# Optimization experiments

Measured on AMD Instinct MI355X. Metric: run time of the kernel, lower is better.

## Reference

```python
import jax, jax.numpy as jnp
import numpy as np

N = 50000          # nodes
E = 800000         # edges (COO)
IN_CH = 128
H1, H2, OUT = 200, 100, 2   # 100*out, 50*out, out with out_channels=2
EPS = 1e-12
DROP_P = 0.1


def setup_inputs() -> dict:
    key = jax.random.key(0)
    ks = jax.random.split(key, 6)
    x = jax.random.normal(ks[0], (N, IN_CH), dtype=jnp.float32)
    edge_index = jax.random.randint(ks[1], (2, E), 0, N)
    W1 = jax.random.normal(ks[2], (IN_CH, H1), dtype=jnp.float32) / np.sqrt(IN_CH)
    W2 = jax.random.normal(ks[3], (H1, H2), dtype=jnp.float32) / np.sqrt(H1)
    W3 = jax.random.normal(ks[4], (H2, OUT), dtype=jnp.float32) / np.sqrt(H2)
    beta1 = jnp.float32(1.0)
    beta2 = jnp.float32(1.0)
    beta3 = jnp.float32(1.0)
    return dict(x=x, edge_index=edge_index, W1=W1, W2=W2, W3=W3,
                beta1=beta1, beta2=beta2, beta3=beta3)


def _agnn_layer(x, W, beta, src, dst):
    # project in -> out channels, then AGNN cosine-attention propagation
    h = x @ W                                               # [N, D]
    hn = h / jnp.maximum(jnp.linalg.norm(h, axis=-1, keepdims=True), EPS)
    a = beta * jnp.sum(hn[src] * hn[dst], axis=-1)          # [E'] edge logits
    amax = jax.ops.segment_max(a, dst, num_segments=N)      # stable segment softmax
    amax = jnp.where(jnp.isfinite(amax), amax, 0.0)
    e = jnp.exp(a - amax[dst])
    denom = jax.ops.segment_sum(e, dst, num_segments=N)
    alpha = e / jnp.maximum(denom[dst], EPS)
    return jax.ops.segment_sum(h[src] * alpha[:, None], dst, num_segments=N)


def _dropout(k, x, p=DROP_P):
    keep = jax.random.bernoulli(k, 1.0 - p, x.shape)
    return jnp.where(keep, x / (1.0 - p), 0.0)


def reference(x, edge_index, W1, W2, W3, beta1, beta2, beta3):
    src, dst = edge_index[0], edge_index[1]
    loop = jnp.arange(N)                                    # self-loops (AGNNConv default)
    src = jnp.concatenate([src, loop])
    dst = jnp.concatenate([dst, loop])
    k1, k2 = jax.random.split(jax.random.key(42))
    h = jax.nn.relu(_agnn_layer(x, W1, beta1, src, dst))
    h = _dropout(k1, h)
    h = jax.nn.relu(_agnn_layer(h, W2, beta2, src, dst))
    h = _dropout(k2, h)
    h = jax.nn.relu(_agnn_layer(h, W3, beta3, src, dst))
    return h
```

## Files before the change

kernel.cpp:

```cpp
#include <hip/hip_runtime.h>
#include <hip/hip_bf16.h>

#define NN 50000
#define NE 800000
#define EPSN 1e-12f


#define H_OFF    0ull
#define A_OFF    40000000ull
#define H3_OFF   80000000ull
#define RINV_OFF 80400000ull
#define OFFS_OFF 80600000ull
#define DEG_OFF  80800016ull
#define CURS_OFF 81000016ull
#define ESRC_OFF 81200016ull
#define CHNK_OFF 84600016ull

__host__ __device__ inline void tf20(unsigned k0, unsigned k1, unsigned& x0, unsigned& x1) {
  unsigned ks2 = k0 ^ k1 ^ 0x1BD11BDAu;
  x0 += k0; x1 += k1;
#define TFR(r) { x0 += x1; x1 = ((x1 << (r)) | (x1 >> (32 - (r)))) ^ x0; }
  TFR(13) TFR(15) TFR(26) TFR(6)
  x0 += k1;  x1 += ks2 + 1u;
  TFR(17) TFR(29) TFR(16) TFR(24)
  x0 += ks2; x1 += k0 + 2u;
  TFR(13) TFR(15) TFR(26) TFR(6)
  x0 += k0;  x1 += k1 + 3u;
  TFR(17) TFR(29) TFR(16) TFR(24)
  x0 += k1;  x1 += ks2 + 4u;
  TFR(13) TFR(15) TFR(26) TFR(6)
  x0 += ks2; x1 += k0 + 5u;
#undef TFR
}

__device__ __forceinline__ float dropf(float val, unsigned k0, unsigned k1, unsigned i) {
  unsigned x0 = 0u, x1 = i;
  tf20(k0, k1, x0, x1);
  unsigned bits = x0 ^ x1;
  float u = __uint_as_float((bits >> 9) | 0x3F800000u) - 1.0f;
  return (u < 0.9f) ? val * (1.0f / 0.9f) : 0.0f;
}

__device__ __forceinline__ float wave_sum(float x) {
  x += __shfl_xor(x, 32); x += __shfl_xor(x, 16); x += __shfl_xor(x, 8);
  x += __shfl_xor(x, 4);  x += __shfl_xor(x, 2);  x += __shfl_xor(x, 1);
  return x;
}

template<int K, int KT, int NLP, int N>
__device__ __forceinline__ void gemm_core(float* __restrict__ As, float* __restrict__ Ws,
                                          const float* __restrict__ A,
                                          const float* __restrict__ W,
                                          float* __restrict__ H,
                                          float* __restrict__ RINV, int M, int row0) {
  static_assert(NLP % 32 == 0, "NLP must be 32-granular");
  constexpr int KTP = KT + 1, NV = N / 4, NC = NLP / 32, CPT = NC * 4;
  const float4* A4 = (const float4*)A;
  const float4* W4 = (const float4*)W;
  const float4* Ws4 = (const float4*)Ws;

  int t = threadIdx.x, rgrp = t >> 3, cg = t & 7;
  float acc0[CPT], acc1[CPT];
#pragma unroll
  for (int j = 0; j < CPT; j++) { acc0[j] = 0.f; acc1[j] = 0.f; }

  for (int k0 = 0; k0 < K; k0 += KT) {
    __syncthreads();
    for (int idx = t; idx < 64 * (KT / 4); idx += 256) {
      int r = idx / (KT / 4), cq = idx - r * (KT / 4);
      int gr = row0 + r;
      float4 v = (gr < M) ? A4[(size_t)gr * (K / 4) + (k0 / 4) + cq]
                          : make_float4(0.f, 0.f, 0.f, 0.f);
      float* dst = &As[r * KTP + cq * 4];
      dst[0] = v.x; dst[1] = v.y; dst[2] = v.z; dst[3] = v.w;
    }
    for (int idx = t; idx < KT * NV; idx += 256) {
      int kk = idx / NV, cq = idx - kk * NV;
      *(float4*)&Ws[kk * NLP + cq * 4] = W4[(size_t)(k0 + kk) * NV + cq];
    }
    if (NLP > N) {
      for (int idx = t; idx < KT * ((NLP - N) / 4); idx += 256) {
        int kk = idx / ((NLP - N) / 4), cq = idx - kk * ((NLP - N) / 4);
        *(float4*)&Ws[kk * NLP + N + cq * 4] = make_float4(0.f, 0.f, 0.f, 0.f);
      }
    }
    __syncthreads();
#pragma unroll
    for (int kk = 0; kk < KT; kk++) {
      float a0 = As[(rgrp * 2) * KTP + kk];
      float a1 = As[(rgrp * 2 + 1) * KTP + kk];
#pragma unroll
      for (int q = 0; q < NC; q++) {
        float4 wv = Ws4[kk * (NLP / 4) + cg + 8 * q];
        acc0[q * 4 + 0] = fmaf(a0, wv.x, acc0[q * 4 + 0]);
        acc0[q * 4 + 1] = fmaf(a0, wv.y, acc0[q * 4 + 1]);
        acc0[q * 4 + 2] = fmaf(a0, wv.z, acc0[q * 4 + 2]);
        acc0[q * 4 + 3] = fmaf(a0, wv.w, acc0[q * 4 + 3]);
        acc1[q * 4 + 0] = fmaf(a1, wv.x, acc1[q * 4 + 0]);
        acc1[q * 4 + 1] = fmaf(a1, wv.y, acc1[q * 4 + 1]);
        acc1[q * 4 + 2] = fmaf(a1, wv.z, acc1[q * 4 + 2]);
        acc1[q * 4 + 3] = fmaf(a1, wv.w, acc1[q * 4 + 3]);
      }
    }
  }

  int r0 = row0 + rgrp * 2;
#pragma unroll
  for (int rr = 0; rr < 2; rr++) {
    int gr = r0 + rr;
    const float* acc = rr ? acc1 : acc0;
    float ss = 0.f;
#pragma unroll
    for (int q = 0; q < NC; q++) {
#pragma unroll
      for (int j = 0; j < 4; j++) {
        float v = acc[q * 4 + j];
        ss += v * v;
        int c = 4 * (cg + 8 * q) + j;
        if (gr < M && c < N) H[(size_t)gr * N + c] = v;
      }
    }
    ss += __shfl_xor(ss, 1); ss += __shfl_xor(ss, 2); ss += __shfl_xor(ss, 4);
    if (cg == 0 && gr < M) RINV[gr] = 1.0f / fmaxf(sqrtf(ss), EPSN);
  }
}

__global__ __launch_bounds__(256) void gemm1_hist_kernel(
    const float* __restrict__ X, const float* __restrict__ W1,
    float* __restrict__ H, float* __restrict__ RINV,
    const int* __restrict__ EI, int* __restrict__ DEG) {
  __shared__ float smem[9280];
  int bid = blockIdx.x;
  if (bid < 782) {
    gemm_core<128, 32, 224, 200>(smem, smem + 2112, X, W1, H, RINV, NN, bid * 64);
  } else {
    for (int e = (bid - 782) * 256 + threadIdx.x; e < NE; e += 242 * 256)
      atomicAdd(&DEG[EI[NE + e]], 1);
  }
}

__global__ __launch_bounds__(256) void csr_scan1_kernel(const int* __restrict__ deg,
                                                        int* __restrict__ offs,
                                                        int* __restrict__ chunk) {
  __shared__ int lds[8];
  int t = threadIdx.x;
  int base = blockIdx.x * 1024 + t * 4;
  int d[4];
#pragma unroll
  for (int j = 0; j < 4; j++) d[j] = (base + j < NN) ? deg[base + j] : 0;
  int ts = d[0] + d[1] + d[2] + d[3];
  int lane = t & 63, wave = t >> 6;
  int inc = ts;
#pragma unroll
  for (int sh = 1; sh < 64; sh <<= 1) { int u = __shfl_up(inc, sh); if (lane >= sh) inc += u; }
  if (lane == 63) lds[wave] = inc;
  __syncthreads();
  if (t == 0) { int s = 0; for (int w = 0; w < 4; w++) { int x = lds[w]; lds[w] = s; s += x; } lds[4] = s; }
  __syncthreads();
  int p = lds[wave] + inc - ts;
#pragma unroll
  for (int j = 0; j < 4; j++) { if (base + j < NN) offs[base + j] = p; p += d[j]; }
  if (t == 255) chunk[blockIdx.x] = lds[4];
}

__global__ __launch_bounds__(64) void csr_scan2_kernel(int* __restrict__ chunk) {
  int t = threadIdx.x;
  int v = (t < 49) ? chunk[t] : 0;
  int inc = v;
#pragma unroll
  for (int sh = 1; sh < 64; sh <<= 1) { int u = __shfl_up(inc, sh); if (t >= sh) inc += u; }
  if (t < 49) chunk[t] = inc - v;
}

__global__ __launch_bounds__(256) void csr_scan3_kernel(int* __restrict__ offs,
                                                        const int* __restrict__ chunk,
                                                        int* __restrict__ curs) {
  int i = blockIdx.x * 256 + threadIdx.x;
  if (i < NN) {
    int val = offs[i] + chunk[i >> 10];
    offs[i] = val;
    curs[i] = val;
  }
  if (i == 0) offs[NN] = NE;
}

__global__ __launch_bounds__(256) void csr_scatter_kernel(const int* __restrict__ ei,
                                                          int* __restrict__ curs,
                                                          int* __restrict__ esrc) {
  int e = blockIdx.x * 256 + threadIdx.x;
  if (e >= NE) return;
  int s = ei[e], d = ei[NE + e];
  int pos = atomicAdd(&curs[d], 1);
  esrc[pos] = s;
}

__global__ __launch_bounds__(256) void gemm2_kernel(const float* A, const float* W,
                                                    float* H, float* RINV, int M) {
  __shared__ float As[64 * 41];
  __shared__ float Ws[40 * 128];
  gemm_core<200, 40, 128, 100>(As, Ws, A, W, H, RINV, M, blockIdx.x * 64);
}

template<int D, int VEC, bool DROP>
__device__ __forceinline__ void attn_body(const float* __restrict__ H,
                                          const float* __restrict__ RINV,
                                          const int* __restrict__ OFFS,
                                          const int* __restrict__ ESRC,
                                          const float* __restrict__ BETA,
                                          float* __restrict__ OUT,
                                          unsigned k0, unsigned k1) {
  constexpr int NL = D / VEC;
  int v = blockIdx.x * 4 + (threadIdx.x >> 6);
  int lane = threadIdx.x & 63;
  bool act = lane < NL;
  float beta = BETA[0];
  float bd = beta * RINV[v];
  int e0 = OFFS[v], e1 = OFFS[v + 1];

  float wself = __expf(beta);
  float s = wself;
  float hd[VEC], acc[VEC];
  if (act) {
    const float* hrow = H + (size_t)v * D + lane * VEC;
    if (VEC == 4) { float4 tv = *(const float4*)hrow; hd[0] = tv.x; hd[1] = tv.y; hd[2] = tv.z; hd[3] = tv.w; }
    else          { float2 tv = *(const float2*)hrow; hd[0] = tv.x; hd[1] = tv.y; }
#pragma unroll
    for (int j = 0; j < VEC; j++) acc[j] = wself * hd[j];
  }

  int idx = e0;
  for (; idx + 4 <= e1; idx += 4) {
    int   u[4];
    float r[4], dt[4], hs[4][VEC];
#pragma unroll
    for (int m = 0; m < 4; m++) u[m] = ESRC[idx + m];
#pragma unroll
    for (int m = 0; m < 4; m++) r[m] = RINV[u[m]];
    float dd[4] = {0.f, 0.f, 0.f, 0.f};
    if (act) {
#pragma unroll
      for (int m = 0; m < 4; m++) {
        const float* p = H + (size_t)u[m] * D + lane * VEC;
        if (VEC == 4) { float4 a = *(const float4*)p; hs[m][0] = a.x; hs[m][1] = a.y; hs[m][2] = a.z; hs[m][3] = a.w; }
        else          { float2 a = *(const float2*)p; hs[m][0] = a.x; hs[m][1] = a.y; }
      }
#pragma unroll
      for (int m = 0; m < 4; m++)
#pragma unroll
        for (int j = 0; j < VEC; j++) dd[m] = fmaf(hd[j], hs[m][j], dd[m]);
    }
#pragma unroll
    for (int m = 0; m < 4; m++) dt[m] = wave_sum(dd[m]);
    float w[4];
#pragma unroll
    for (int m = 0; m < 4; m++) { w[m] = __expf(bd * dt[m] * r[m]); s += w[m]; }
    if (act) {
#pragma unroll
      for (int m = 0; m < 4; m++)
#pragma unroll
        for (int j = 0; j < VEC; j++) acc[j] = fmaf(w[m], hs[m][j], acc[j]);
    }
  }
  for (; idx < e1; ++idx) {
    int u0 = ESRC[idx];
    float r0 = RINV[u0];
    float h0[VEC];
    float ddt = 0.f;
    if (act) {
      const float* p0 = H + (size_t)u0 * D + lane * VEC;
      if (VEC == 4) { float4 a = *(const float4*)p0; h0[0] = a.x; h0[1] = a.y; h0[2] = a.z; h0[3] = a.w; }
      else          { float2 a = *(const float2*)p0; h0[0] = a.x; h0[1] = a.y; }
#pragma unroll
      for (int j = 0; j < VEC; j++) ddt = fmaf(hd[j], h0[j], ddt);
    }
    ddt = wave_sum(ddt);
    float w0 = __expf(bd * ddt * r0);
    s += w0;
    if (act) {
#pragma unroll
      for (int j = 0; j < VEC; j++) acc[j] = fmaf(w0, h0[j], acc[j]);
    }
  }

  float rs = 1.0f / fmaxf(s, EPSN);
  if (act) {
    float o[VEC];
#pragma unroll
    for (int j = 0; j < VEC; j++) {
      float val = acc[j] * rs;
      val = (val <= 0.0f) ? 0.0f : val;
      if (DROP) val = dropf(val, k0, k1, (unsigned)(v * D + lane * VEC + j));
      o[j] = val;
    }
    float* orow = OUT + (size_t)v * D + lane * VEC;
    if (VEC == 4) *(float4*)orow = make_float4(o[0], o[1], o[2], o[3]);
    else          *(float2*)orow = make_float2(o[0], o[1]);
  }
}

__global__ __launch_bounds__(256) void attn1_kernel(const float* H, const float* RINV,
                                                    const int* OFFS, const int* ESRC,
                                                    const float* BETA, float* OUT,
                                                    unsigned k0, unsigned k1) {
  attn_body<200, 4, true>(H, RINV, OFFS, ESRC, BETA, OUT, k0, k1);
}
__global__ __launch_bounds__(256) void attn2_kernel(const float* H, const float* RINV,
                                                    const int* OFFS, const int* ESRC,
                                                    const float* BETA, float* OUT,
                                                    unsigned k0, unsigned k1) {
  attn_body<100, 2, true>(H, RINV, OFFS, ESRC, BETA, OUT, k0, k1);
}

__global__ __launch_bounds__(256) void gemm3_kernel(const float* __restrict__ A2,
                                                    const float* __restrict__ W3,
                                                    float* __restrict__ H3,
                                                    float* __restrict__ RINV) {
  __shared__ float w3s[200];
  for (int i = threadIdx.x; i < 200; i += 256) w3s[i] = W3[i];
  __syncthreads();
  int v = blockIdx.x * 256 + threadIdx.x;
  if (v >= NN) return;
  const float* row = A2 + (size_t)v * 100;
  float o0 = 0.f, o1 = 0.f;
#pragma unroll 4
  for (int k = 0; k < 100; k++) {
    float x = row[k];
    o0 = fmaf(x, w3s[2 * k], o0);
    o1 = fmaf(x, w3s[2 * k + 1], o1);
  }
  H3[2 * v] = o0; H3[2 * v + 1] = o1;
  RINV[v] = 1.0f / fmaxf(sqrtf(o0 * o0 + o1 * o1), EPSN);
}

__global__ __launch_bounds__(256) void attn3_kernel(const float* __restrict__ H3,
                                                    const float* __restrict__ RINV,
                                                    const int* __restrict__ OFFS,
                                                    const int* __restrict__ ESRC,
                                                    const float* __restrict__ BETA,
                                                    float* __restrict__ out) {
  int v = blockIdx.x * 4 + (threadIdx.x >> 6);
  int lane = threadIdx.x & 63;
  float beta = BETA[0];
  float bd = beta * RINV[v];
  float h0 = H3[2 * v], h1 = H3[2 * v + 1];
  int e0 = OFFS[v], e1 = OFFS[v + 1];
  float s = 0.f, a0 = 0.f, a1 = 0.f;
  for (int idx = e0 + lane; idx < e1; idx += 64) {
    int u = ESRC[idx];
    float s0 = H3[2 * u], s1 = H3[2 * u + 1];
    float w = __expf(bd * (h0 * s0 + h1 * s1) * RINV[u]);
    s += w; a0 = fmaf(w, s0, a0); a1 = fmaf(w, s1, a1);
  }
  s = wave_sum(s); a0 = wave_sum(a0); a1 = wave_sum(a1);
  if (lane == 0) {
    float wself = __expf(beta);
    s += wself; a0 = fmaf(wself, h0, a0); a1 = fmaf(wself, h1, a1);
    float rs = 1.0f / fmaxf(s, EPSN);
    float o0 = a0 * rs, o1 = a1 * rs;
    out[2 * v]     = (o0 <= 0.0f) ? 0.0f : o0;
    out[2 * v + 1] = (o1 <= 0.0f) ? 0.0f : o1;
  }
}

extern "C" void kernel_launch(void* const* d_in, const int* in_sizes, int n_in,
                              void* d_out, int out_size, void* d_ws, size_t ws_size,
                              hipStream_t stream) {
  const float* X  = (const float*)d_in[0];
  const int*   EI = (const int*)d_in[1];
  const float* W1 = (const float*)d_in[2];
  const float* W2 = (const float*)d_in[3];
  const float* W3 = (const float*)d_in[4];
  const float* B1 = (const float*)d_in[5];
  const float* B2 = (const float*)d_in[6];
  const float* B3 = (const float*)d_in[7];

  char* ws = (char*)d_ws;
  float* H    = (float*)(ws + H_OFF);
  float* A    = (float*)(ws + A_OFF);
  float* H3   = (float*)(ws + H3_OFF);
  float* RINV = (float*)(ws + RINV_OFF);
  int* OFFS   = (int*)(ws + OFFS_OFF);
  int* DEG    = (int*)(ws + DEG_OFF);
  int* CURS   = (int*)(ws + CURS_OFF);
  int* ESRC   = (int*)(ws + ESRC_OFF);
  int* CHNK   = (int*)(ws + CHNK_OFF);

  unsigned k1a = 0u, k1b = 0u; tf20(0u, 42u, k1a, k1b);
  unsigned k2a = 0u, k2b = 1u; tf20(0u, 42u, k2a, k2b);

  hipMemsetAsync(DEG, 0, NN * sizeof(int), stream);

  gemm1_hist_kernel<<<1024, 256, 0, stream>>>(X, W1, H, RINV, EI, DEG);
  csr_scan1_kernel<<<49, 256, 0, stream>>>(DEG, OFFS, CHNK);
  csr_scan2_kernel<<<1, 64, 0, stream>>>(CHNK);
  csr_scan3_kernel<<<196, 256, 0, stream>>>(OFFS, CHNK, CURS);
  csr_scatter_kernel<<<(NE + 255) / 256, 256, 0, stream>>>(EI, CURS, ESRC);

  const int gb = (NN + 63) / 64;
  const int ab = NN / 4;

  attn1_kernel<<<ab, 256, 0, stream>>>(H, RINV, OFFS, ESRC, B1, A, k1a, k1b);
  gemm2_kernel<<<gb, 256, 0, stream>>>(A, W2, H, RINV, NN);
  attn2_kernel<<<ab, 256, 0, stream>>>(H, RINV, OFFS, ESRC, B2, A, k2a, k2b);
  gemm3_kernel<<<(NN + 255) / 256, 256, 0, stream>>>(A, W3, H3, RINV);
  attn3_kernel<<<ab, 256, 0, stream>>>(H3, RINV, OFFS, ESRC, B3, (float*)d_out);
}
```

Baseline: 491.6 us.

## Stage full A rows in LDS and read weights directly from global cache

The GEMM core now loads each block's whole 64-row A tile into LDS once, with 16B-aligned padded rows, instead of looping over K tiles with two syncs per step. The weight tile is no longer staged in LDS; each thread reads W float4 values straight from global memory and relies on the cache, since W is small and shared by all blocks. Launch bounds are set to request four blocks per CU. This removes the per-tile barriers and LDS traffic for W, but adds repeated global/L2 loads of W inside the inner loop and a larger LDS footprint per block.

```diff
diff --git a/kernel.cpp b/kernel.cpp
--- a/kernel.cpp
+++ b/kernel.cpp
@@ -47,60 +47,54 @@
   return x;
 }
 
-template<int K, int KT, int NLP, int N>
-__device__ __forceinline__ void gemm_core(float* __restrict__ As, float* __restrict__ Ws,
-                                          const float* __restrict__ A,
-                                          const float* __restrict__ W,
-                                          float* __restrict__ H,
-                                          float* __restrict__ RINV, int M, int row0) {
-  static_assert(NLP % 32 == 0, "NLP must be 32-granular");
-  constexpr int KTP = KT + 1, NV = N / 4, NC = NLP / 32, CPT = NC * 4;
+template<int K, int KTP, int N, int NC>
+__device__ __forceinline__ void gemm_core_gw(float* __restrict__ As,
+                                             const float* __restrict__ A,
+                                             const float* __restrict__ W,
+                                             float* __restrict__ H,
+                                             float* __restrict__ RINV, int M, int row0) {
+  constexpr int NV = N / 4;
+  static_assert(KTP % 4 == 0, "KTP must keep rows 16B-aligned");
   const float4* A4 = (const float4*)A;
   const float4* W4 = (const float4*)W;
-  const float4* Ws4 = (const float4*)Ws;
 
   int t = threadIdx.x, rgrp = t >> 3, cg = t & 7;
-  float acc0[CPT], acc1[CPT];
-#pragma unroll
-  for (int j = 0; j < CPT; j++) { acc0[j] = 0.f; acc1[j] = 0.f; }
-
-  for (int k0 = 0; k0 < K; k0 += KT) {
-    __syncthreads();
-    for (int idx = t; idx < 64 * (KT / 4); idx += 256) {
-      int r = idx / (KT / 4), cq = idx - r * (KT / 4);
-      int gr = row0 + r;
-      float4 v = (gr < M) ? A4[(size_t)gr * (K / 4) + (k0 / 4) + cq]
-                          : make_float4(0.f, 0.f, 0.f, 0.f);
-      float* dst = &As[r * KTP + cq * 4];
-      dst[0] = v.x; dst[1] = v.y; dst[2] = v.z; dst[3] = v.w;
-    }
-    for (int idx = t; idx < KT * NV; idx += 256) {
-      int kk = idx / NV, cq = idx - kk * NV;
-      *(float4*)&Ws[kk * NLP + cq * 4] = W4[(size_t)(k0 + kk) * NV + cq];
-    }
-    if (NLP > N) {
-      for (int idx = t; idx < KT * ((NLP - N) / 4); idx += 256) {
-        int kk = idx / ((NLP - N) / 4), cq = idx - kk * ((NLP - N) / 4);
-        *(float4*)&Ws[kk * NLP + N + cq * 4] = make_float4(0.f, 0.f, 0.f, 0.f);
-      }
-    }
-    __syncthreads();
-#pragma unroll
-    for (int kk = 0; kk < KT; kk++) {
-      float a0 = As[(rgrp * 2) * KTP + kk];
-      float a1 = As[(rgrp * 2 + 1) * KTP + kk];
-#pragma unroll
-      for (int q = 0; q < NC; q++) {
-        float4 wv = Ws4[kk * (NLP / 4) + cg + 8 * q];
-        acc0[q * 4 + 0] = fmaf(a0, wv.x, acc0[q * 4 + 0]);
-        acc0[q * 4 + 1] = fmaf(a0, wv.y, acc0[q * 4 + 1]);
-        acc0[q * 4 + 2] = fmaf(a0, wv.z, acc0[q * 4 + 2]);
-        acc0[q * 4 + 3] = fmaf(a0, wv.w, acc0[q * 4 + 3]);
-        acc1[q * 4 + 0] = fmaf(a1, wv.x, acc1[q * 4 + 0]);
-        acc1[q * 4 + 1] = fmaf(a1, wv.y, acc1[q * 4 + 1]);
-        acc1[q * 4 + 2] = fmaf(a1, wv.z, acc1[q * 4 + 2]);
-        acc1[q * 4 + 3] = fmaf(a1, wv.w, acc1[q * 4 + 3]);
-      }
+
+  for (int idx = t; idx < 64 * (K / 4); idx += 256) {
+    int r = idx / (K / 4), cq = idx - r * (K / 4);
+    int gr = row0 + r;
+    float4 v = (gr < M) ? A4[(size_t)gr * (K / 4) + cq]
+                        : make_float4(0.f, 0.f, 0.f, 0.f);
+    *(float4*)&As[r * KTP + cq * 4] = v;
+  }
+
+  int ci[NC], cw[NC];
+#pragma unroll
+  for (int q = 0; q < NC; q++) { ci[q] = cg + 8 * q; cw[q] = (ci[q] < NV) ? ci[q] : 0; }
+
+  float acc0[NC * 4], acc1[NC * 4];
+#pragma unroll
+  for (int j = 0; j < NC * 4; j++) { acc0[j] = 0.f; acc1[j] = 0.f; }
+
+  __syncthreads();
+
+  const float* As0 = &As[(rgrp * 2) * KTP];
+  const float* As1 = &As[(rgrp * 2 + 1) * KTP];
+#pragma unroll 2
+  for (int kk = 0; kk < K; kk++) {
+    float a0 = As0[kk];
+    float a1 = As1[kk];
+#pragma unroll
+    for (int q = 0; q < NC; q++) {
+      float4 wv = W4[kk * NV + cw[q]];
+      acc0[q * 4 + 0] = fmaf(a0, wv.x, acc0[q * 4 + 0]);
+      acc0[q * 4 + 1] = fmaf(a0, wv.y, acc0[q * 4 + 1]);
+      acc0[q * 4 + 2] = fmaf(a0, wv.z, acc0[q * 4 + 2]);
+      acc0[q * 4 + 3] = fmaf(a0, wv.w, acc0[q * 4 + 3]);
+      acc1[q * 4 + 0] = fmaf(a1, wv.x, acc1[q * 4 + 0]);
+      acc1[q * 4 + 1] = fmaf(a1, wv.y, acc1[q * 4 + 1]);
+      acc1[q * 4 + 2] = fmaf(a1, wv.z, acc1[q * 4 + 2]);
+      acc1[q * 4 + 3] = fmaf(a1, wv.w, acc1[q * 4 + 3]);
     }
   }
 
@@ -115,9 +109,11 @@
 #pragma unroll
       for (int j = 0; j < 4; j++) {
         float v = acc[q * 4 + j];
-        ss += v * v;
-        int c = 4 * (cg + 8 * q) + j;
-        if (gr < M && c < N) H[(size_t)gr * N + c] = v;
+        int c = 4 * ci[q] + j;
+        if (c < N) {
+          ss += v * v;
+          if (gr < M) H[(size_t)gr * N + c] = v;
+        }
       }
     }
     ss += __shfl_xor(ss, 1); ss += __shfl_xor(ss, 2); ss += __shfl_xor(ss, 4);
@@ -125,18 +121,26 @@
   }
 }
 
-__global__ __launch_bounds__(256) void gemm1_hist_kernel(
+__global__ __launch_bounds__(256, 4) void gemm1_hist_kernel(
     const float* __restrict__ X, const float* __restrict__ W1,
     float* __restrict__ H, float* __restrict__ RINV,
     const int* __restrict__ EI, int* __restrict__ DEG) {
-  __shared__ float smem[9280];
+  __shared__ float As[64 * 132];
   int bid = blockIdx.x;
   if (bid < 782) {
-    gemm_core<128, 32, 224, 200>(smem, smem + 2112, X, W1, H, RINV, NN, bid * 64);
+    gemm_core_gw<128, 132, 200, 7>(As, X, W1, H, RINV, NN, bid * 64);
   } else {
     for (int e = (bid - 782) * 256 + threadIdx.x; e < NE; e += 242 * 256)
       atomicAdd(&DEG[EI[NE + e]], 1);
   }
+}
+
+__global__ __launch_bounds__(256, 4) void gemm2_kernel(const float* __restrict__ A,
+                                                       const float* __restrict__ W,
+                                                       float* __restrict__ H,
+                                                       float* __restrict__ RINV, int M) {
+  __shared__ float As[64 * 204];
+  gemm_core_gw<200, 204, 100, 4>(As, A, W, H, RINV, M, blockIdx.x * 64);
 }
 
 __global__ __launch_bounds__(256) void csr_scan1_kernel(const int* __restrict__ deg,
@@ -192,13 +196,6 @@
   int s = ei[e], d = ei[NE + e];
   int pos = atomicAdd(&curs[d], 1);
   esrc[pos] = s;
-}
-
-__global__ __launch_bounds__(256) void gemm2_kernel(const float* A, const float* W,
-                                                    float* H, float* RINV, int M) {
-  __shared__ float As[64 * 41];
-  __shared__ float Ws[40 * 128];
-  gemm_core<200, 40, 128, 100>(As, Ws, A, W, H, RINV, M, blockIdx.x * 64);
 }
 
 template<int D, int VEC, bool DROP>
```

New measurement: 583.9 us. 18.8% more time.
